# Kernel optimization log

Hardware: AMD Instinct MI355X
Metric: run time of the kernel (lower is better)

The kernel has to match this reference:

```python
import jax, jax.numpy as jnp
import numpy as np

INPUT_LAYER_SIZE = 40960 * 2
LAYER1_SIZE = 512
LAYER2_SIZE = 32
LAYER3_SIZE = 32
BATCH = 4096


def setup_inputs() -> dict:
    key = jax.random.key(0)
    ks = jax.random.split(key, 10)
    # Sparse one-hot style features: mostly zeros with ~30 active entries per side.
    def sparse_features(k, n_active=30):
        kidx, = jax.random.split(k, 1)
        idx = jax.random.randint(kidx, (BATCH, n_active), 0, 40960)
        feats = jnp.zeros((BATCH, 40960), dtype=jnp.float32)
        return feats.at[jnp.arange(BATCH)[:, None], idx].set(1.0)
    w_features = sparse_features(ks[0])
    b_features = sparse_features(ks[1])
    s_in = 1.0 / np.sqrt(INPUT_LAYER_SIZE)
    s1 = 1.0 / np.sqrt(LAYER1_SIZE)
    s2 = 1.0 / np.sqrt(LAYER2_SIZE)
    s3 = 1.0 / np.sqrt(LAYER3_SIZE)
    return {
        "w_features": w_features,
        "b_features": b_features,
        "W_in": jax.random.uniform(ks[2], (LAYER1_SIZE, INPUT_LAYER_SIZE), jnp.float32, -s_in, s_in),
        "b_in": jax.random.uniform(ks[3], (LAYER1_SIZE,), jnp.float32, -s_in, s_in),
        "W1": jax.random.uniform(ks[4], (LAYER2_SIZE, LAYER1_SIZE), jnp.float32, -s1, s1),
        "b1": jax.random.uniform(ks[5], (LAYER2_SIZE,), jnp.float32, -s1, s1),
        "W2": jax.random.uniform(ks[6], (LAYER3_SIZE, LAYER2_SIZE), jnp.float32, -s2, s2),
        "b2": jax.random.uniform(ks[7], (LAYER3_SIZE,), jnp.float32, -s2, s2),
        "W3": jax.random.uniform(ks[8], (1, LAYER3_SIZE), jnp.float32, -s3, s3),
        "b3": jax.random.uniform(ks[9], (1,), jnp.float32, -s3, s3),
    }


def reference(w_features, b_features, W_in, b_in, W1, b1, W2, b2, W3, b3):
    # Concatenate both perspectives: [B, 81920]
    x = jnp.concatenate([w_features, b_features], axis=1)
    # Huge sparse-input accumulator layer (the kernel-headroom op)
    accum = x @ W_in.T + b_in                       # [B, 512]
    l1 = jnp.clip(accum, 0.0, 1.0)                  # clipped ReLU
    l2 = jnp.clip(l1 @ W1.T + b1, 0.0, 1.0)         # [B, 32]
    l3 = jnp.clip(l2 @ W2.T + b2, 0.0, 1.0)         # [B, 32]
    return l3 @ W3.T + b3                           # [B, 1]
```

## Files before the change

kernel.cpp:

```cpp
#include <hip/hip_runtime.h>
#include <hip/hip_bf16.h>

#define IN_PER_SIDE   40960
#define IN_TOTAL      81920
#define L1            512
#define L2            32
#define L3_           32
#define BATCH         4096
#define MAXIDX        128

typedef float        v4f __attribute__((ext_vector_type(4)));
typedef float        v8f __attribute__((ext_vector_type(8)));
typedef _Float16     v4h __attribute__((ext_vector_type(4)));
typedef _Float16     v8h __attribute__((ext_vector_type(8)));
typedef unsigned int v4u __attribute__((ext_vector_type(4)));

#define WT_BYTES ((size_t)IN_TOTAL * L1 * sizeof(_Float16))

__global__ __launch_bounds__(256) void transpose_win(
    const float* __restrict__ W, _Float16* __restrict__ WTh)
{
    __shared__ float tile[64][65];
    const int jt = blockIdx.x * 64;
    const int ot = blockIdx.y * 64;

    {
        const int tx = threadIdx.x & 15;
        const int ty = threadIdx.x >> 4;
#pragma unroll
        for (int k = 0; k < 4; ++k) {
            const int o = ty + 16 * k;
            const v4f* p = (const v4f*)&W[(size_t)(ot + o) * IN_TOTAL + jt + 4 * tx];
            v4f v = __builtin_nontemporal_load(p);
            tile[4 * tx + 0][o] = v.x;
            tile[4 * tx + 1][o] = v.y;
            tile[4 * tx + 2][o] = v.z;
            tile[4 * tx + 3][o] = v.w;
        }
    }
    __syncthreads();
    {
        const int tx = threadIdx.x & 7;
        const int ty = threadIdx.x >> 3;
#pragma unroll
        for (int k = 0; k < 2; ++k) {
            const int j = ty + 32 * k;
            v8f v;
#pragma unroll
            for (int c = 0; c < 8; ++c) v[c] = tile[j][8 * tx + c];
            v8h h = __builtin_convertvector(v, v8h);
            *(v8h*)&WTh[(size_t)(jt + j) * L1 + ot + 8 * tx] = h;
        }
    }
}

__global__ __launch_bounds__(512) void nnue_fused(
    const float* __restrict__ wf, const float* __restrict__ bfeat,
    const _Float16* __restrict__ WTh,
    const float* __restrict__ b_in,
    const float* __restrict__ W1, const float* __restrict__ b1,
    const float* __restrict__ W2, const float* __restrict__ b2,
    const float* __restrict__ W3, const float* __restrict__ b3,
    float* __restrict__ out)
{
    const int b = blockIdx.x;
    const int t = threadIdx.x;

    __shared__ int   sidx[MAXIDX];
    __shared__ int   scnt;
    __shared__ float accs[8 * 64 * 9];
    __shared__ float l1s[L1];
    __shared__ float l2acc[L2];
    __shared__ float l2s[L2];
    __shared__ float l3s[L3_];

    if (t == 0) { scnt = 0; sidx[0] = 0; }
    __syncthreads();

    const v4u* wrow = (const v4u*)(wf    + (size_t)b * IN_PER_SIDE);
    const v4u* brow = (const v4u*)(bfeat + (size_t)b * IN_PER_SIDE);
    const int nvec = IN_PER_SIDE / 4;

    v4u vw = __builtin_nontemporal_load(wrow + t);
    v4u vb = __builtin_nontemporal_load(brow + t);
    for (int i = t; ; ) {
        const int inext = i + 512;
        const bool more = inext < nvec;
        v4u nw, nb;
        if (more) {
            nw = __builtin_nontemporal_load(wrow + inext);
            nb = __builtin_nontemporal_load(brow + inext);
        }
        if (vw.x | vw.y | vw.z | vw.w) {
            if (vw.x) sidx[atomicAdd(&scnt, 1)] = 4 * i + 0;
            if (vw.y) sidx[atomicAdd(&scnt, 1)] = 4 * i + 1;
            if (vw.z) sidx[atomicAdd(&scnt, 1)] = 4 * i + 2;
            if (vw.w) sidx[atomicAdd(&scnt, 1)] = 4 * i + 3;
        }
        if (vb.x | vb.y | vb.z | vb.w) {
            if (vb.x) sidx[atomicAdd(&scnt, 1)] = IN_PER_SIDE + 4 * i + 0;
            if (vb.y) sidx[atomicAdd(&scnt, 1)] = IN_PER_SIDE + 4 * i + 1;
            if (vb.z) sidx[atomicAdd(&scnt, 1)] = IN_PER_SIDE + 4 * i + 2;
            if (vb.w) sidx[atomicAdd(&scnt, 1)] = IN_PER_SIDE + 4 * i + 3;
        }
        if (!more) break;
        i = inext; vw = nw; vb = nb;
    }
    __syncthreads();

    const int n = scnt;
    const int w = t >> 6;
    const int l = t & 63;
    const v8h* WTH8 = (const v8h*)WTh;

    v8f acc0 = {0, 0, 0, 0, 0, 0, 0, 0};
    v8f acc1 = {0, 0, 0, 0, 0, 0, 0, 0};
    const int J     = (n + 7) >> 3;
    const int Jeven = (J + 1) & ~1;

    {
        const int f0 = w, f1 = w + 8;
        v8h h0 = WTH8[(size_t)sidx[f0 < n ? f0 : 0] * 64 + l];
        float s0 = (f0 < n) ? 1.0f : 0.0f;
        v8h h1 = WTH8[(size_t)sidx[f1 < n ? f1 : 0] * 64 + l];
        float s1 = (f1 < n) ? 1.0f : 0.0f;
        for (int j = 2; j < Jeven; j += 2) {
            const int g0 = w + 8 * j, g1 = g0 + 8;
            v8h p0 = WTH8[(size_t)sidx[g0 < n ? g0 : 0] * 64 + l];
            const float u0 = (g0 < n) ? 1.0f : 0.0f;
            v8h p1 = WTH8[(size_t)sidx[g1 < n ? g1 : 0] * 64 + l];
            const float u1 = (g1 < n) ? 1.0f : 0.0f;
            acc0 += s0 * __builtin_convertvector(h0, v8f);
            acc1 += s1 * __builtin_convertvector(h1, v8f);
            h0 = p0; s0 = u0; h1 = p1; s1 = u1;
        }
        acc0 += s0 * __builtin_convertvector(h0, v8f);
        acc1 += s1 * __builtin_convertvector(h1, v8f);
    }
    acc0 += acc1;

    {
        float* dst = &accs[(w * 64 + l) * 9];
#pragma unroll
        for (int i = 0; i < 8; ++i) dst[i] = acc0[i];
    }
    __syncthreads();

    {
        const int ll = t >> 3, c = t & 7;
        float s = 0.0f;
#pragma unroll
        for (int ww = 0; ww < 8; ++ww) s += accs[(ww * 64 + ll) * 9 + c];
        l1s[t] = fminf(fmaxf(s + b_in[t], 0.0f), 1.0f);
    }
    __syncthreads();

    {
        const int kk = t >> 4;
        const int gg = t & 15;
        const float* wp = W1 + (size_t)kk * L1;
        float p = 0.0f;
        for (int o = gg; o < L1; o += 16) p += wp[o] * l1s[o];
#pragma unroll
        for (int off = 8; off > 0; off >>= 1) p += __shfl_down(p, off, 16);
        if (gg == 0) l2acc[kk] = p;
    }
    __syncthreads();
    if (t < L2) l2s[t] = fminf(fmaxf(l2acc[t] + b1[t], 0.0f), 1.0f);
    __syncthreads();

    if (t < L3_) {
        const float* wp = W2 + (size_t)t * L2;
        float p = b2[t];
#pragma unroll
        for (int q = 0; q < L2; ++q) p += wp[q] * l2s[q];
        l3s[t] = fminf(fmaxf(p, 0.0f), 1.0f);
    }
    __syncthreads();

    if (t == 0) {
        float p = b3[0];
#pragma unroll
        for (int q = 0; q < L3_; ++q) p += W3[q] * l3s[q];
        out[b] = p;
    }
}

__global__ __launch_bounds__(512) void nnue_fallback(
    const float* __restrict__ wf, const float* __restrict__ bfeat,
    const float* __restrict__ W_in, const float* __restrict__ b_in,
    const float* __restrict__ W1, const float* __restrict__ b1,
    const float* __restrict__ W2, const float* __restrict__ b2,
    const float* __restrict__ W3, const float* __restrict__ b3,
    float* __restrict__ out)
{
    const int b = blockIdx.x;
    const int t = threadIdx.x;
    __shared__ int   idxs[MAXIDX];
    __shared__ int   scnt;
    __shared__ float l1s[L1];
    __shared__ float l2acc[L2];
    __shared__ float l2s[L2];
    __shared__ float l3s[L3_];

    if (t == 0) scnt = 0;
    __syncthreads();
    const v4f* wrow = (const v4f*)(wf    + (size_t)b * IN_PER_SIDE);
    const v4f* brow = (const v4f*)(bfeat + (size_t)b * IN_PER_SIDE);
    for (int i = t; i < IN_PER_SIDE / 4; i += 512) {
        v4f v = wrow[i];
        if (v.x != 0.0f) idxs[atomicAdd(&scnt, 1)] = 4 * i + 0;
        if (v.y != 0.0f) idxs[atomicAdd(&scnt, 1)] = 4 * i + 1;
        if (v.z != 0.0f) idxs[atomicAdd(&scnt, 1)] = 4 * i + 2;
        if (v.w != 0.0f) idxs[atomicAdd(&scnt, 1)] = 4 * i + 3;
        v4f u = brow[i];
        if (u.x != 0.0f) idxs[atomicAdd(&scnt, 1)] = IN_PER_SIDE + 4 * i + 0;
        if (u.y != 0.0f) idxs[atomicAdd(&scnt, 1)] = IN_PER_SIDE + 4 * i + 1;
        if (u.z != 0.0f) idxs[atomicAdd(&scnt, 1)] = IN_PER_SIDE + 4 * i + 2;
        if (u.w != 0.0f) idxs[atomicAdd(&scnt, 1)] = IN_PER_SIDE + 4 * i + 3;
    }
    __syncthreads();
    const int n = scnt;
    float a0 = 0.0f;
    const float* row = W_in + (size_t)t * IN_TOTAL;
    for (int i = 0; i < n; ++i) a0 += row[idxs[i]];
    l1s[t] = fminf(fmaxf(b_in[t] + a0, 0.0f), 1.0f);
    __syncthreads();
    {
        const int k = t >> 4, g = t & 15;
        const float* wp = W1 + (size_t)k * L1;
        float p = 0.0f;
        for (int o = g; o < L1; o += 16) p += wp[o] * l1s[o];
#pragma unroll
        for (int off = 8; off > 0; off >>= 1) p += __shfl_down(p, off, 16);
        if (g == 0) l2acc[k] = p;
    }
    __syncthreads();
    if (t < L2) l2s[t] = fminf(fmaxf(l2acc[t] + b1[t], 0.0f), 1.0f);
    __syncthreads();
    if (t < L3_) {
        const float* wp = W2 + (size_t)t * L2;
        float p = b2[t];
#pragma unroll
        for (int q = 0; q < L2; ++q) p += wp[q] * l2s[q];
        l3s[t] = fminf(fmaxf(p, 0.0f), 1.0f);
    }
    __syncthreads();
    if (t == 0) {
        float p = b3[0];
#pragma unroll
        for (int q = 0; q < L3_; ++q) p += W3[q] * l3s[q];
        out[b] = p;
    }
}

extern "C" void kernel_launch(void* const* d_in, const int* in_sizes, int n_in,
                              void* d_out, int out_size, void* d_ws, size_t ws_size,
                              hipStream_t stream) {
    const float* wf   = (const float*)d_in[0];
    const float* bfeat= (const float*)d_in[1];
    const float* W_in = (const float*)d_in[2];
    const float* b_in = (const float*)d_in[3];
    const float* W1   = (const float*)d_in[4];
    const float* b1   = (const float*)d_in[5];
    const float* W2   = (const float*)d_in[6];
    const float* b2   = (const float*)d_in[7];
    const float* W3   = (const float*)d_in[8];
    const float* b3   = (const float*)d_in[9];
    float* out = (float*)d_out;

    if (ws_size >= WT_BYTES) {
        _Float16* WTh = (_Float16*)d_ws;
        dim3 grid(IN_TOTAL / 64, L1 / 64);
        transpose_win<<<grid, 256, 0, stream>>>(W_in, WTh);
        nnue_fused<<<BATCH, 512, 0, stream>>>(
            wf, bfeat, WTh, b_in, W1, b1, W2, b2, W3, b3, out);
    } else {
        nnue_fallback<<<BATCH, 512, 0, stream>>>(
            wf, bfeat, W_in, b_in, W1, b1, W2, b2, W3, b3, out);
    }
}
```

Measured before the change: 1.326 ms.

## Move sparse feature index extraction into the weight-transpose prep kernel

The scan of the dense feature rows for nonzero entries moves out of the per-row fused kernel and into the transpose kernel. Each of the 10240 prep blocks now also scans a slice of both feature matrices and appends indices to per-row global lists using global atomics. The fused kernel then only loads a precomputed index list, so the two bandwidth-bound phases run concurrently in one grid rather than serially. The cost is an extra zeroing launch, global atomics, and unordered index lists.

```diff
diff --git a/kernel.cpp b/kernel.cpp
--- a/kernel.cpp
+++ b/kernel.cpp
@@ -16,13 +16,23 @@
 typedef unsigned int v4u __attribute__((ext_vector_type(4)));
 
 #define WT_BYTES ((size_t)IN_TOTAL * L1 * sizeof(_Float16))
-
-__global__ __launch_bounds__(256) void transpose_win(
-    const float* __restrict__ W, _Float16* __restrict__ WTh)
+#define CNT_OFF  WT_BYTES
+#define IDX_OFF  (WT_BYTES + 16384)
+#define WS_NEED  (IDX_OFF + (size_t)BATCH * MAXIDX * 4)
+
+__global__ __launch_bounds__(256) void zero_cnt(int* __restrict__ cnt)
+{
+    cnt[blockIdx.x * 256 + threadIdx.x] = 0;
+}
+
+__global__ __launch_bounds__(256) void prep(
+    const float* __restrict__ W, _Float16* __restrict__ WTh,
+    const float* __restrict__ wf, const float* __restrict__ bfeat,
+    int* __restrict__ cnt, int* __restrict__ idxg)
 {
     __shared__ float tile[64][65];
-    const int jt = blockIdx.x * 64;
-    const int ot = blockIdx.y * 64;
+    const int jt = (blockIdx.x % 1280) * 64;
+    const int ot = (blockIdx.x / 1280) * 64;
 
     {
         const int tx = threadIdx.x & 15;
@@ -52,11 +62,39 @@
             *(v8h*)&WTh[(size_t)(jt + j) * L1 + ot + 8 * tx] = h;
         }
     }
+
+    const v4u* wv = (const v4u*)wf;
+    const v4u* bv = (const v4u*)bfeat;
+    const size_t base = (size_t)blockIdx.x * 4096 + threadIdx.x;
+#pragma unroll 4
+    for (int u = 0; u < 16; ++u) {
+        const size_t i = base + (size_t)u * 256;
+        const v4u a = __builtin_nontemporal_load(wv + i);
+        const v4u c = __builtin_nontemporal_load(bv + i);
+        if (a.x | a.y | a.z | a.w) {
+            const int row = (int)(i / 10240);
+            const int fb  = (int)(i % 10240) * 4;
+            int* lst = idxg + (size_t)row * MAXIDX;
+            if (a.x) { int p = atomicAdd(&cnt[row], 1); if (p < MAXIDX) lst[p] = fb + 0; }
+            if (a.y) { int p = atomicAdd(&cnt[row], 1); if (p < MAXIDX) lst[p] = fb + 1; }
+            if (a.z) { int p = atomicAdd(&cnt[row], 1); if (p < MAXIDX) lst[p] = fb + 2; }
+            if (a.w) { int p = atomicAdd(&cnt[row], 1); if (p < MAXIDX) lst[p] = fb + 3; }
+        }
+        if (c.x | c.y | c.z | c.w) {
+            const int row = (int)(i / 10240);
+            const int fb  = IN_PER_SIDE + (int)(i % 10240) * 4;
+            int* lst = idxg + (size_t)row * MAXIDX;
+            if (c.x) { int p = atomicAdd(&cnt[row], 1); if (p < MAXIDX) lst[p] = fb + 0; }
+            if (c.y) { int p = atomicAdd(&cnt[row], 1); if (p < MAXIDX) lst[p] = fb + 1; }
+            if (c.z) { int p = atomicAdd(&cnt[row], 1); if (p < MAXIDX) lst[p] = fb + 2; }
+            if (c.w) { int p = atomicAdd(&cnt[row], 1); if (p < MAXIDX) lst[p] = fb + 3; }
+        }
+    }
 }
 
 __global__ __launch_bounds__(512) void nnue_fused(
-    const float* __restrict__ wf, const float* __restrict__ bfeat,
     const _Float16* __restrict__ WTh,
+    const int* __restrict__ cnt, const int* __restrict__ idxg,
     const float* __restrict__ b_in,
     const float* __restrict__ W1, const float* __restrict__ b1,
     const float* __restrict__ W2, const float* __restrict__ b2,
@@ -67,48 +105,19 @@
     const int t = threadIdx.x;
 
     __shared__ int   sidx[MAXIDX];
-    __shared__ int   scnt;
     __shared__ float accs[8 * 64 * 9];
     __shared__ float l1s[L1];
     __shared__ float l2acc[L2];
     __shared__ float l2s[L2];
     __shared__ float l3s[L3_];
 
-    if (t == 0) { scnt = 0; sidx[0] = 0; }
-    __syncthreads();
-
-    const v4u* wrow = (const v4u*)(wf    + (size_t)b * IN_PER_SIDE);
-    const v4u* brow = (const v4u*)(bfeat + (size_t)b * IN_PER_SIDE);
-    const int nvec = IN_PER_SIDE / 4;
-
-    v4u vw = __builtin_nontemporal_load(wrow + t);
-    v4u vb = __builtin_nontemporal_load(brow + t);
-    for (int i = t; ; ) {
-        const int inext = i + 512;
-        const bool more = inext < nvec;
-        v4u nw, nb;
-        if (more) {
-            nw = __builtin_nontemporal_load(wrow + inext);
-            nb = __builtin_nontemporal_load(brow + inext);
-        }
-        if (vw.x | vw.y | vw.z | vw.w) {
-            if (vw.x) sidx[atomicAdd(&scnt, 1)] = 4 * i + 0;
-            if (vw.y) sidx[atomicAdd(&scnt, 1)] = 4 * i + 1;
-            if (vw.z) sidx[atomicAdd(&scnt, 1)] = 4 * i + 2;
-            if (vw.w) sidx[atomicAdd(&scnt, 1)] = 4 * i + 3;
-        }
-        if (vb.x | vb.y | vb.z | vb.w) {
-            if (vb.x) sidx[atomicAdd(&scnt, 1)] = IN_PER_SIDE + 4 * i + 0;
-            if (vb.y) sidx[atomicAdd(&scnt, 1)] = IN_PER_SIDE + 4 * i + 1;
-            if (vb.z) sidx[atomicAdd(&scnt, 1)] = IN_PER_SIDE + 4 * i + 2;
-            if (vb.w) sidx[atomicAdd(&scnt, 1)] = IN_PER_SIDE + 4 * i + 3;
-        }
-        if (!more) break;
-        i = inext; vw = nw; vb = nb;
-    }
-    __syncthreads();
-
-    const int n = scnt;
+    const int n = min(cnt[b], MAXIDX);
+    if (t < MAXIDX) {
+        const int g = idxg[(size_t)b * MAXIDX + t];
+        sidx[t] = (t < n) ? g : 0;
+    }
+    __syncthreads();
+
     const int w = t >> 6;
     const int l = t & 63;
     const v8h* WTH8 = (const v8h*)WTh;
@@ -269,12 +278,15 @@
     const float* b3   = (const float*)d_in[9];
     float* out = (float*)d_out;
 
-    if (ws_size >= WT_BYTES) {
-        _Float16* WTh = (_Float16*)d_ws;
-        dim3 grid(IN_TOTAL / 64, L1 / 64);
-        transpose_win<<<grid, 256, 0, stream>>>(W_in, WTh);
+    if (ws_size >= WS_NEED) {
+        char* ws = (char*)d_ws;
+        _Float16* WTh = (_Float16*)ws;
+        int* cnt  = (int*)(ws + CNT_OFF);
+        int* idxg = (int*)(ws + IDX_OFF);
+        zero_cnt<<<BATCH / 256, 256, 0, stream>>>(cnt);
+        prep<<<10240, 256, 0, stream>>>(W_in, WTh, wf, bfeat, cnt, idxg);
         nnue_fused<<<BATCH, 512, 0, stream>>>(
-            wf, bfeat, WTh, b_in, W1, b1, W2, b2, W3, b3, out);
+            WTh, cnt, idxg, b_in, W1, b1, W2, b2, W3, b3, out);
     } else {
         nnue_fallback<<<BATCH, 512, 0, stream>>>(
             wf, bfeat, W_in, b_in, W1, b1, W2, b2, W3, b3, out);
```

Result: slower. 1.400 ms (+5.6%).
